# Optimization experiments

Measured on AMD Instinct MI355X. Metric: run time of the kernel, lower is better.

Reference implementation:

```python
import jax, jax.numpy as jnp
import numpy as np

EMBED_DIM = 512
N_QUERY = 4096
N_PROTO = 1024


def setup_inputs() -> dict:
    key = jax.random.key(0)
    k_q, k_p, k_wmu = jax.random.split(key, 3)
    d = EMBED_DIM
    bound = (6.0 / (d + d)) ** 0.5
    return {
        "query_features": jax.random.normal(k_q, (N_QUERY, d), dtype=jnp.float32),
        "prototypes": jax.random.normal(k_p, (N_PROTO, d), dtype=jnp.float32),
        "weight_mu": jax.random.uniform(k_wmu, (d, d), dtype=jnp.float32, minval=-bound, maxval=bound),
        "weight_rho": jnp.full((d, d), -3.0, dtype=jnp.float32),
        "bias_mu": jnp.zeros((d,), dtype=jnp.float32),
        "bias_rho": jnp.full((d,), 0.01, dtype=jnp.float32),
        "n_samples": 10,
    }


def reference(query_features, prototypes, weight_mu, weight_rho, bias_mu, bias_rho, n_samples):
    d = weight_mu.shape[0]
    # softplus reparameterization (same each iteration in the original loop)
    weight_sigma = jnp.log1p(jnp.exp(weight_rho))  # [d, d]
    bias_sigma = jnp.log1p(jnp.exp(bias_rho))      # [d]
    # batched MC weight/bias samples: [S, d, d] and [S, d]
    key = jax.random.key(42)
    kw, kb = jax.random.split(key)
    eps_w = jax.random.normal(kw, (n_samples, d, d), dtype=weight_mu.dtype)
    eps_b = jax.random.normal(kb, (n_samples, d), dtype=bias_mu.dtype)
    w = weight_mu[None] + weight_sigma[None] * eps_w   # [S, d, d]
    b = bias_mu[None] + bias_sigma[None] * eps_b       # [S, d]
    # F.linear(x, W_sample.T, b) == x @ W_sample + b
    tq = jnp.einsum('qd,sde->sqe', query_features, w) + b[:, None, :]  # [S, Q, d]
    # cdist via ||a||^2 + ||b||^2 - 2 a.b
    sq_q = jnp.sum(tq * tq, axis=-1)                    # [S, Q]
    sq_p = jnp.sum(prototypes * prototypes, axis=-1)    # [P]
    cross = jnp.einsum('sqe,pe->sqp', tq, prototypes)   # [S, Q, P]
    sqd = sq_q[:, :, None] + sq_p[None, None, :] - 2.0 * cross
    dists = jnp.sqrt(jnp.maximum(sqd, 1e-12))           # [S, Q, P]
    mean_distance = jnp.mean(dists, axis=0)
    uncertainty = jnp.std(dists, axis=0, ddof=1)        # torch.std is unbiased
    return mean_distance, uncertainty
```

## Files before the change

kernel.cpp:

```cpp
#include <hip/hip_runtime.h>
#include <stdint.h>

#define NS 10
#define DIM 512
#define NQ 4096
#define NP 1024

typedef unsigned short ushort_t;
typedef __bf16 bf16el_t;
typedef bf16el_t bf16x8 __attribute__((ext_vector_type(8)));
typedef float floatx4 __attribute__((ext_vector_type(4)));

__host__ __device__ __forceinline__ uint32_t rotl32(uint32_t x, int r) {
  return (x << r) | (x >> (32 - r));
}

__host__ __device__ __forceinline__ void threefry2x32(uint32_t k0, uint32_t k1,
                                                      uint32_t x0, uint32_t x1,
                                                      uint32_t* o0, uint32_t* o1) {
  uint32_t ks2 = k0 ^ k1 ^ 0x1BD11BDAu;
  x0 += k0; x1 += k1;
#define TF_R(r) { x0 += x1; x1 = rotl32(x1, r); x1 ^= x0; }
  TF_R(13) TF_R(15) TF_R(26) TF_R(6)   x0 += k1;  x1 += ks2 + 1u;
  TF_R(17) TF_R(29) TF_R(16) TF_R(24)  x0 += ks2; x1 += k0 + 2u;
  TF_R(13) TF_R(15) TF_R(26) TF_R(6)   x0 += k0;  x1 += k1 + 3u;
  TF_R(17) TF_R(29) TF_R(16) TF_R(24)  x0 += k1;  x1 += ks2 + 4u;
  TF_R(13) TF_R(15) TF_R(26) TF_R(6)   x0 += ks2; x1 += k0 + 5u;
#undef TF_R
  *o0 = x0; *o1 = x1;
}

__device__ __forceinline__ uint32_t jax_random_bits(uint32_t k0, uint32_t k1, uint32_t idx) {
  uint32_t o0, o1;
  threefry2x32(k0, k1, 0u, idx, &o0, &o1);
  return o0 ^ o1;
}

__device__ __forceinline__ float erfinvf_xla(float x) {
  float w = -log1pf(-x * x);
  float p;
  if (w < 5.0f) {
    w -= 2.5f;
    p = 2.81022636e-08f;
    p = fmaf(p, w, 3.43273939e-07f);
    p = fmaf(p, w, -3.5233877e-06f);
    p = fmaf(p, w, -4.39150654e-06f);
    p = fmaf(p, w, 0.00021858087f);
    p = fmaf(p, w, -0.00125372503f);
    p = fmaf(p, w, -0.00417768164f);
    p = fmaf(p, w, 0.246640727f);
    p = fmaf(p, w, 1.50140941f);
  } else {
    w = sqrtf(w) - 3.0f;
    p = -0.000200214257f;
    p = fmaf(p, w, 0.000100950558f);
    p = fmaf(p, w, 0.00134934322f);
    p = fmaf(p, w, -0.00367342844f);
    p = fmaf(p, w, 0.00573950773f);
    p = fmaf(p, w, -0.0076224613f);
    p = fmaf(p, w, 0.00943887047f);
    p = fmaf(p, w, 1.00167406f);
    p = fmaf(p, w, 2.83297682f);
  }
  return p * x;
}

__device__ __forceinline__ float jax_bits_to_normal(uint32_t bits) {
  float f = __uint_as_float((bits >> 9) | 0x3F800000u) - 1.0f;
  float u = f * 2.0f - 0.99999994f;
  u = fmaxf(u, -0.99999994f);
  return 1.41421356f * erfinvf_xla(u);
}

__device__ __forceinline__ float softplusf(float x) { return log1pf(expf(x)); }

__device__ __forceinline__ float bf2f(ushort_t u) {
  return __uint_as_float(((uint32_t)u) << 16);
}
__device__ __forceinline__ ushort_t f2bf(float f) {
  uint32_t u = __float_as_uint(f);
  u += 0x7FFFu + ((u >> 16) & 1u);
  return (ushort_t)(u >> 16);
}

__device__ __forceinline__ void gll16(const void* g, void* l) {
  __builtin_amdgcn_global_load_lds(
      (const __attribute__((address_space(1))) uint32_t*)g,
      (__attribute__((address_space(3))) uint32_t*)l, 16, 0, 0);
}


__global__ __launch_bounds__(256) void gen_w_kernel(const float* __restrict__ wmu,
                                                    const float* __restrict__ wrho,
                                                    ushort_t* __restrict__ wt,
                                                    uint32_t kw0, uint32_t kw1) {
  uint32_t tid = blockIdx.x * 256u + threadIdx.x;
  uint32_t s = tid >> 18;
  uint32_t r = tid & 0x3FFFFu;
  uint32_t e = r >> 9;
  uint32_t k = r & 511u;
  uint32_t eps_idx = (s << 18) | (k << 9) | e;
  uint32_t bits = jax_random_bits(kw0, kw1, eps_idx);
  float n = jax_bits_to_normal(bits);
  uint32_t mi = (k << 9) | e;
  float w = wmu[mi] + softplusf(wrho[mi]) * n;
  wt[tid] = f2bf(w);
}

__global__ __launch_bounds__(256) void gen_b_kernel(const float* __restrict__ bmu,
                                                    const float* __restrict__ brho,
                                                    float* __restrict__ bvec,
                                                    uint32_t kb0, uint32_t kb1) {
  uint32_t tid = blockIdx.x * 256u + threadIdx.x;
  uint32_t e = tid & 511u;
  uint32_t bits = jax_random_bits(kb0, kb1, tid);
  float n = jax_bits_to_normal(bits);
  bvec[tid] = bmu[e] + softplusf(brho[e]) * n;
}

__global__ __launch_bounds__(256) void cvt_q_kernel(const float* __restrict__ qf,
                                                    ushort_t* __restrict__ qb) {
  int i = (blockIdx.x * 256 + threadIdx.x) * 4;
  float4 v = *(const float4*)&qf[i];
  uint2 r;
  r.x = (uint32_t)f2bf(v.x) | ((uint32_t)f2bf(v.y) << 16);
  r.y = (uint32_t)f2bf(v.z) | ((uint32_t)f2bf(v.w) << 16);
  *(uint2*)&qb[i] = r;
}

__global__ __launch_bounds__(64) void cvt_p_sqp_kernel(const float* __restrict__ pf,
                                                       ushort_t* __restrict__ pb,
                                                       float* __restrict__ sqp) {
  int p = blockIdx.x;
  int lane = threadIdx.x;
  const float* src = pf + p * DIM + lane * 8;
  float4 a = *(const float4*)src;
  float4 b = *(const float4*)(src + 4);
  float vals[8] = {a.x, a.y, a.z, a.w, b.x, b.y, b.z, b.w};
  ushort_t o[8];
  float ss = 0.f;
#pragma unroll
  for (int i = 0; i < 8; ++i) {
    o[i] = f2bf(vals[i]);
    float f = bf2f(o[i]);
    ss += f * f;
  }
  *(uint4*)&pb[p * DIM + lane * 8] = *(const uint4*)o;
#pragma unroll
  for (int off = 32; off; off >>= 1) ss += __shfl_xor(ss, off, 64);
  if (lane == 0) sqp[p] = ss;
}


__global__ __launch_bounds__(256) void gemm_tq_kernel(const ushort_t* __restrict__ qb,
                                                      const ushort_t* __restrict__ wt,
                                                      const float* __restrict__ bvec,
                                                      ushort_t* __restrict__ tq) {
  __shared__ __align__(16) ushort_t lsA[128 * 64];
  __shared__ __align__(16) ushort_t lsB[128 * 64];
  const int lane = threadIdx.x & 63;
  const int wave = threadIdx.x >> 6;
  const int wm = wave >> 1, wn = wave & 1;
  const int qBase = blockIdx.x * 128;
  const int eBase = blockIdx.y * 128;
  const int s = blockIdx.z;
  const ushort_t* wbase = wt + (size_t)s * (DIM * DIM);
  const int srow = lane >> 3;
  const int scol = ((lane & 7) ^ srow) * 16;
  const char* gA = (const char*)qb + (size_t)(qBase + wave * 32 + srow) * (DIM * 2) + scol;
  const char* gB = (const char*)wbase + (size_t)(eBase + wave * 32 + srow) * (DIM * 2) + scol;
  char* lA = (char*)&lsA[wave * 32 * 64];
  char* lB = (char*)&lsB[wave * 32 * 64];
  const int cn = lane & 15;
  const int cn7 = cn & 7;
  const int jc = lane >> 4;
  const floatx4 fzero = {0.f, 0.f, 0.f, 0.f};
  floatx4 acc[4][4];
#pragma unroll
  for (int mi = 0; mi < 4; ++mi)
#pragma unroll
    for (int ni = 0; ni < 4; ++ni) acc[mi][ni] = fzero;

  for (int kt = 0; kt < 8; ++kt) {
    __syncthreads();
#pragma unroll
    for (int j = 0; j < 4; ++j) {
      gll16(gA + (size_t)j * 8 * (DIM * 2), lA + j * 1024);
      gll16(gB + (size_t)j * 8 * (DIM * 2), lB + j * 1024);
    }
    gA += 128; gB += 128;
    __syncthreads();
#pragma unroll
    for (int c = 0; c < 8; c += 4) {
      const int po = ((c + jc) ^ cn7) << 3;
      bf16x8 aF[4], bF[4];
#pragma unroll
      for (int mi = 0; mi < 4; ++mi)
        aF[mi] = *(const bf16x8*)&lsA[(wm * 64 + mi * 16 + cn) * 64 + po];
#pragma unroll
      for (int ni = 0; ni < 4; ++ni)
        bF[ni] = *(const bf16x8*)&lsB[(wn * 64 + ni * 16 + cn) * 64 + po];
#pragma unroll
      for (int mi = 0; mi < 4; ++mi)
#pragma unroll
        for (int ni = 0; ni < 4; ++ni)
          acc[mi][ni] = __builtin_amdgcn_mfma_f32_16x16x32_bf16(aF[mi], bF[ni], acc[mi][ni], 0, 0, 0);
    }
  }
  const int rq = (lane >> 4) * 4;
#pragma unroll
  for (int ni = 0; ni < 4; ++ni) {
    const int e = eBase + wn * 64 + ni * 16 + cn;
    const float bv = bvec[s * DIM + e];
#pragma unroll
    for (int mi = 0; mi < 4; ++mi)
#pragma unroll
      for (int r = 0; r < 4; ++r) {
        const int q = qBase + wm * 64 + mi * 16 + rq + r;
        tq[(size_t)s * (NQ * DIM) + (size_t)q * DIM + e] = f2bf(acc[mi][ni][r] + bv);
      }
  }
}

__global__ __launch_bounds__(256) void sqq_kernel(const ushort_t* __restrict__ tq,
                                                  float* __restrict__ sqq) {
  int tid = blockIdx.x * 256 + threadIdx.x;
  int row = tid >> 4;
  int sub = tid & 15;
  const uint4* rp = (const uint4*)(tq + (size_t)row * DIM);
  float ss = 0.f;
#pragma unroll
  for (int i = 0; i < 4; ++i) {
    uint4 v = rp[sub + i * 16];
    uint32_t wsv[4] = {v.x, v.y, v.z, v.w};
#pragma unroll
    for (int j = 0; j < 4; ++j) {
      float lo = bf2f((ushort_t)(wsv[j] & 0xFFFFu));
      float hi = bf2f((ushort_t)(wsv[j] >> 16));
      ss += lo * lo + hi * hi;
    }
  }
#pragma unroll
  for (int off = 8; off; off >>= 1) ss += __shfl_xor(ss, off, 64);
  if (sub == 0) sqq[row] = ss;
}

__global__ __launch_bounds__(256) void gemm_dist_kernel(const ushort_t* __restrict__ tq,
                                                        const ushort_t* __restrict__ pb,
                                                        const float* __restrict__ sqq,
                                                        const float* __restrict__ sqp,
                                                        float* __restrict__ out) {
  __shared__ __align__(16) ushort_t lsA[64 * 64];
  __shared__ __align__(16) ushort_t lsB[128 * 64];
  const int lane = threadIdx.x & 63;
  const int wave = threadIdx.x >> 6;
  const int wm = wave >> 1;
  const int wn = wave & 1;
  const int qBase = blockIdx.x * 64;
  const int pBase = blockIdx.y * 128;
  const int srow = lane >> 3;
  const int scol = ((lane & 7) ^ srow) * 16;
  const char* gA = (const char*)tq + (size_t)(qBase + wave * 16 + srow) * (DIM * 2) + scol;
  const char* gB = (const char*)pb + (size_t)(pBase + wave * 32 + srow) * (DIM * 2) + scol;
  char* lA = (char*)&lsA[wave * 16 * 64];
  char* lB = (char*)&lsB[wave * 32 * 64];
  const int cn = lane & 15;
  const int cn7 = cn & 7;
  const int jc = lane >> 4;
  const int rq = (lane >> 4) * 4;
  const floatx4 fzero = {0.f, 0.f, 0.f, 0.f};

  float sum[2][4][4] = {};
  float ssq[2][4][4] = {};
  float sqp_v[4];
#pragma unroll
  for (int ni = 0; ni < 4; ++ni) sqp_v[ni] = sqp[pBase + wn * 64 + ni * 16 + cn];

  for (int s = 0; s < NS; ++s) {
    floatx4 acc[2][4];
#pragma unroll
    for (int mi = 0; mi < 2; ++mi)
#pragma unroll
      for (int ni = 0; ni < 4; ++ni) acc[mi][ni] = fzero;

    for (int kt = 0; kt < 8; ++kt) {
      __syncthreads();
      gll16(gA, lA);
      gll16(gA + (size_t)8 * (DIM * 2), lA + 1024);
#pragma unroll
      for (int j = 0; j < 4; ++j)
        gll16(gB + (size_t)j * 8 * (DIM * 2), lB + j * 1024);
      gA += 128; gB += 128;
      __syncthreads();
#pragma unroll
      for (int c = 0; c < 8; c += 4) {
        const int po = ((c + jc) ^ cn7) << 3;
        bf16x8 aF[2], bF[4];
#pragma unroll
        for (int mi = 0; mi < 2; ++mi)
          aF[mi] = *(const bf16x8*)&lsA[(wm * 32 + mi * 16 + cn) * 64 + po];
#pragma unroll
        for (int ni = 0; ni < 4; ++ni)
          bF[ni] = *(const bf16x8*)&lsB[(wn * 64 + ni * 16 + cn) * 64 + po];
#pragma unroll
        for (int mi = 0; mi < 2; ++mi)
#pragma unroll
          for (int ni = 0; ni < 4; ++ni)
            acc[mi][ni] = __builtin_amdgcn_mfma_f32_16x16x32_bf16(aF[mi], bF[ni], acc[mi][ni], 0, 0, 0);
      }
    }
    gA += (size_t)NQ * DIM * 2 - 1024;
    gB -= 1024;
#pragma unroll
    for (int mi = 0; mi < 2; ++mi) {
      float4 aqv = *(const float4*)&sqq[s * NQ + qBase + wm * 32 + mi * 16 + rq];
      float aqa[4] = {aqv.x, aqv.y, aqv.z, aqv.w};
#pragma unroll
      for (int r = 0; r < 4; ++r) {
        float aq = aqa[r];
#pragma unroll
        for (int ni = 0; ni < 4; ++ni) {
          float c = acc[mi][ni][r];
          float dd = sqrtf(fmaxf(aq + sqp_v[ni] - 2.0f * c, 1e-12f));
          sum[mi][ni][r] += dd;
          ssq[mi][ni][r] += dd * dd;
        }
      }
    }
  }
#pragma unroll
  for (int mi = 0; mi < 2; ++mi)
#pragma unroll
    for (int ni = 0; ni < 4; ++ni)
#pragma unroll
      for (int r = 0; r < 4; ++r) {
        int q = qBase + wm * 32 + mi * 16 + rq + r;
        int p = pBase + wn * 64 + ni * 16 + cn;
        float sm = sum[mi][ni][r];
        float mean = sm * 0.1f;
        float var = (ssq[mi][ni][r] - sm * sm * 0.1f) * (1.0f / 9.0f);
        out[(size_t)q * NP + p] = mean;
        out[(size_t)NQ * NP + (size_t)q * NP + p] = sqrtf(fmaxf(var, 0.0f));
      }
}

extern "C" void kernel_launch(void* const* d_in, const int* in_sizes, int n_in,
                              void* d_out, int out_size, void* d_ws, size_t ws_size,
                              hipStream_t stream) {
  const float* qf   = (const float*)d_in[0];
  const float* pf   = (const float*)d_in[1];
  const float* wmu  = (const float*)d_in[2];
  const float* wrho = (const float*)d_in[3];
  const float* bmu  = (const float*)d_in[4];
  const float* brho = (const float*)d_in[5];
  float* out = (float*)d_out;
  char* ws = (char*)d_ws;
  ushort_t* wt   = (ushort_t*)(ws);
  ushort_t* qb   = (ushort_t*)(ws + 5242880);
  ushort_t* pb   = (ushort_t*)(ws + 9437184);
  float*    bvec = (float*)   (ws + 10485760);
  float*    sqp  = (float*)   (ws + 10506240);
  ushort_t* tq   = (ushort_t*)(ws + 10510336);
  float*    sqq  = (float*)   (ws + 52453376);

  uint32_t kw0, kw1, kb0, kb1;
  threefry2x32(0u, 42u, 0u, 0u, &kw0, &kw1);
  threefry2x32(0u, 42u, 0u, 1u, &kb0, &kb1);

  hipLaunchKernelGGL(gen_w_kernel, dim3(10240), dim3(256), 0, stream, wmu, wrho, wt, kw0, kw1);
  hipLaunchKernelGGL(gen_b_kernel, dim3(20), dim3(256), 0, stream, bmu, brho, bvec, kb0, kb1);
  hipLaunchKernelGGL(cvt_q_kernel, dim3(2048), dim3(256), 0, stream, qf, qb);
  hipLaunchKernelGGL(cvt_p_sqp_kernel, dim3(1024), dim3(64), 0, stream, pf, pb, sqp);
  hipLaunchKernelGGL(gemm_tq_kernel, dim3(32, 4, 10), dim3(256), 0, stream, qb, wt, bvec, tq);
  hipLaunchKernelGGL(sqq_kernel, dim3(2560), dim3(256), 0, stream, tq, sqq);
  hipLaunchKernelGGL(gemm_dist_kernel, dim3(64, 8), dim3(256), 0, stream, tq, pb, sqq, sqp, out);
}
```

Baseline: 226.2 us.

## Fuse prep kernels, fold row norms into GEMM epilogue, widen dist K-tile

Merges the bias generation, query/prototype conversion and sqq zeroing into a single prep kernel, which cuts launch count. The tq GEMM epilogue now stages its output tile through swizzled LDS, writes tq with coalesced 16-byte stores, and accumulates the squared row norms with atomics, so the separate sqq pass over tq is gone. The distance GEMM doubles its K tile to 128 with a 16-chunk swizzle, halving the number of barrier iterations at the cost of more LDS. It also accumulates sqd directly instead of squaring the sqrt. The risks are atomic contention across the four e-blocks and lower occupancy from the larger LDS footprint.

```diff
diff --git a/kernel.cpp b/kernel.cpp
--- a/kernel.cpp
+++ b/kernel.cpp
@@ -89,7 +89,6 @@
       (__attribute__((address_space(3))) uint32_t*)l, 16, 0, 0);
 }
 
-
 __global__ __launch_bounds__(256) void gen_w_kernel(const float* __restrict__ wmu,
                                                     const float* __restrict__ wrho,
                                                     ushort_t* __restrict__ wt,
@@ -107,57 +106,64 @@
   wt[tid] = f2bf(w);
 }
 
-__global__ __launch_bounds__(256) void gen_b_kernel(const float* __restrict__ bmu,
-                                                    const float* __restrict__ brho,
-                                                    float* __restrict__ bvec,
-                                                    uint32_t kb0, uint32_t kb1) {
-  uint32_t tid = blockIdx.x * 256u + threadIdx.x;
-  uint32_t e = tid & 511u;
-  uint32_t bits = jax_random_bits(kb0, kb1, tid);
-  float n = jax_bits_to_normal(bits);
-  bvec[tid] = bmu[e] + softplusf(brho[e]) * n;
-}
-
-__global__ __launch_bounds__(256) void cvt_q_kernel(const float* __restrict__ qf,
-                                                    ushort_t* __restrict__ qb) {
-  int i = (blockIdx.x * 256 + threadIdx.x) * 4;
-  float4 v = *(const float4*)&qf[i];
-  uint2 r;
-  r.x = (uint32_t)f2bf(v.x) | ((uint32_t)f2bf(v.y) << 16);
-  r.y = (uint32_t)f2bf(v.z) | ((uint32_t)f2bf(v.w) << 16);
-  *(uint2*)&qb[i] = r;
-}
-
-__global__ __launch_bounds__(64) void cvt_p_sqp_kernel(const float* __restrict__ pf,
-                                                       ushort_t* __restrict__ pb,
-                                                       float* __restrict__ sqp) {
-  int p = blockIdx.x;
-  int lane = threadIdx.x;
-  const float* src = pf + p * DIM + lane * 8;
-  float4 a = *(const float4*)src;
-  float4 b = *(const float4*)(src + 4);
-  float vals[8] = {a.x, a.y, a.z, a.w, b.x, b.y, b.z, b.w};
-  ushort_t o[8];
-  float ss = 0.f;
-#pragma unroll
-  for (int i = 0; i < 8; ++i) {
-    o[i] = f2bf(vals[i]);
-    float f = bf2f(o[i]);
-    ss += f * f;
-  }
-  *(uint4*)&pb[p * DIM + lane * 8] = *(const uint4*)o;
-#pragma unroll
-  for (int off = 32; off; off >>= 1) ss += __shfl_xor(ss, off, 64);
-  if (lane == 0) sqp[p] = ss;
-}
-
+__global__ __launch_bounds__(256) void prep_kernel(const float* __restrict__ qf,
+                                                   const float* __restrict__ pf,
+                                                   const float* __restrict__ bmu,
+                                                   const float* __restrict__ brho,
+                                                   ushort_t* __restrict__ qb,
+                                                   ushort_t* __restrict__ pb,
+                                                   float* __restrict__ sqp,
+                                                   float* __restrict__ bvec,
+                                                   float* __restrict__ sqq,
+                                                   uint32_t kb0, uint32_t kb1) {
+  const int blk = blockIdx.x;
+  const int tid = threadIdx.x;
+  if (blk < 2048) {
+    int i = (blk * 256 + tid) * 4;
+    float4 v = *(const float4*)&qf[i];
+    uint2 r;
+    r.x = (uint32_t)f2bf(v.x) | ((uint32_t)f2bf(v.y) << 16);
+    r.y = (uint32_t)f2bf(v.z) | ((uint32_t)f2bf(v.w) << 16);
+    *(uint2*)&qb[i] = r;
+  } else if (blk < 2304) {
+    int p = (blk - 2048) * 4 + (tid >> 6);
+    int lane = tid & 63;
+    const float* src = pf + p * DIM + lane * 8;
+    float4 a = *(const float4*)src;
+    float4 b = *(const float4*)(src + 4);
+    float vals[8] = {a.x, a.y, a.z, a.w, b.x, b.y, b.z, b.w};
+    ushort_t o[8];
+    float ss = 0.f;
+#pragma unroll
+    for (int i = 0; i < 8; ++i) {
+      o[i] = f2bf(vals[i]);
+      float f = bf2f(o[i]);
+      ss += f * f;
+    }
+    *(uint4*)&pb[p * DIM + lane * 8] = *(const uint4*)o;
+#pragma unroll
+    for (int off = 32; off; off >>= 1) ss += __shfl_xor(ss, off, 64);
+    if (lane == 0) sqp[p] = ss;
+  } else if (blk < 2324) {
+    uint32_t t2 = (blk - 2304) * 256u + tid;
+    uint32_t e = t2 & 511u;
+    uint32_t bits = jax_random_bits(kb0, kb1, t2);
+    float n = jax_bits_to_normal(bits);
+    bvec[t2] = bmu[e] + softplusf(brho[e]) * n;
+  } else {
+    int i = (blk - 2324) * 256 + tid;
+    sqq[i] = 0.f;
+  }
+}
 
 __global__ __launch_bounds__(256) void gemm_tq_kernel(const ushort_t* __restrict__ qb,
                                                       const ushort_t* __restrict__ wt,
                                                       const float* __restrict__ bvec,
-                                                      ushort_t* __restrict__ tq) {
-  __shared__ __align__(16) ushort_t lsA[128 * 64];
-  __shared__ __align__(16) ushort_t lsB[128 * 64];
+                                                      ushort_t* __restrict__ tq,
+                                                      float* __restrict__ sqq) {
+  __shared__ __align__(16) ushort_t ls[2 * 128 * 64];
+  ushort_t* lsA = ls;
+  ushort_t* lsB = ls + 128 * 64;
   const int lane = threadIdx.x & 63;
   const int wave = threadIdx.x >> 6;
   const int wm = wave >> 1, wn = wave & 1;
@@ -207,42 +213,48 @@
           acc[mi][ni] = __builtin_amdgcn_mfma_f32_16x16x32_bf16(aF[mi], bF[ni], acc[mi][ni], 0, 0, 0);
     }
   }
-  const int rq = (lane >> 4) * 4;
-#pragma unroll
-  for (int ni = 0; ni < 4; ++ni) {
-    const int e = eBase + wn * 64 + ni * 16 + cn;
-    const float bv = bvec[s * DIM + e];
-#pragma unroll
-    for (int mi = 0; mi < 4; ++mi)
+
+  __syncthreads();
+  ushort_t* area = ls + wave * 4096;
+  float bv[4];
+#pragma unroll
+  for (int ni = 0; ni < 4; ++ni) bv[ni] = bvec[s * DIM + eBase + wn * 64 + ni * 16 + cn];
+  const int jc4 = jc * 4;
+#pragma unroll
+  for (int mi = 0; mi < 4; ++mi)
+#pragma unroll
+    for (int ni = 0; ni < 4; ++ni)
 #pragma unroll
       for (int r = 0; r < 4; ++r) {
-        const int q = qBase + wm * 64 + mi * 16 + rq + r;
-        tq[(size_t)s * (NQ * DIM) + (size_t)q * DIM + e] = f2bf(acc[mi][ni][r] + bv);
+        const int lr = mi * 16 + jc4 + r;
+        const int lc = ni * 16 + cn;
+        const int off = lr * 64 + (((lc >> 3) ^ (lr & 7)) << 3) + (lc & 7);
+        area[off] = f2bf(acc[mi][ni][r] + bv[ni]);
       }
-  }
-}
-
-__global__ __launch_bounds__(256) void sqq_kernel(const ushort_t* __restrict__ tq,
-                                                  float* __restrict__ sqq) {
-  int tid = blockIdx.x * 256 + threadIdx.x;
-  int row = tid >> 4;
-  int sub = tid & 15;
-  const uint4* rp = (const uint4*)(tq + (size_t)row * DIM);
-  float ss = 0.f;
-#pragma unroll
-  for (int i = 0; i < 4; ++i) {
-    uint4 v = rp[sub + i * 16];
+  __syncthreads();
+  const int rr = lane >> 3;
+  const int ch = lane & 7;
+  const int physc = ch ^ rr;
+  const size_t tqs = (size_t)s * (NQ * DIM);
+#pragma unroll
+  for (int pass = 0; pass < 8; ++pass) {
+    const int lr = pass * 8 + rr;
+    uint4 v = *(const uint4*)&area[lr * 64 + physc * 8];
     uint32_t wsv[4] = {v.x, v.y, v.z, v.w};
-#pragma unroll
-    for (int j = 0; j < 4; ++j) {
-      float lo = bf2f((ushort_t)(wsv[j] & 0xFFFFu));
-      float hi = bf2f((ushort_t)(wsv[j] >> 16));
+    float ss = 0.f;
+#pragma unroll
+    for (int i = 0; i < 4; ++i) {
+      float lo = bf2f((ushort_t)(wsv[i] & 0xFFFFu));
+      float hi = bf2f((ushort_t)(wsv[i] >> 16));
       ss += lo * lo + hi * hi;
     }
-  }
-#pragma unroll
-  for (int off = 8; off; off >>= 1) ss += __shfl_xor(ss, off, 64);
-  if (sub == 0) sqq[row] = ss;
+    ss += __shfl_xor(ss, 1, 64);
+    ss += __shfl_xor(ss, 2, 64);
+    ss += __shfl_xor(ss, 4, 64);
+    const int q = qBase + wm * 64 + lr;
+    *(uint4*)&tq[tqs + (size_t)q * DIM + eBase + wn * 64 + ch * 8] = v;
+    if (ch == 0) atomicAdd(&sqq[s * NQ + q], ss);
+  }
 }
 
 __global__ __launch_bounds__(256) void gemm_dist_kernel(const ushort_t* __restrict__ tq,
@@ -250,24 +262,24 @@
                                                         const float* __restrict__ sqq,
                                                         const float* __restrict__ sqp,
                                                         float* __restrict__ out) {
-  __shared__ __align__(16) ushort_t lsA[64 * 64];
-  __shared__ __align__(16) ushort_t lsB[128 * 64];
+  __shared__ __align__(16) ushort_t lsA[64 * 128];
+  __shared__ __align__(16) ushort_t lsB[128 * 128];
   const int lane = threadIdx.x & 63;
   const int wave = threadIdx.x >> 6;
   const int wm = wave >> 1;
   const int wn = wave & 1;
   const int qBase = blockIdx.x * 64;
   const int pBase = blockIdx.y * 128;
-  const int srow = lane >> 3;
-  const int scol = ((lane & 7) ^ srow) * 16;
-  const char* gA = (const char*)tq + (size_t)(qBase + wave * 16 + srow) * (DIM * 2) + scol;
-  const char* gB = (const char*)pb + (size_t)(pBase + wave * 32 + srow) * (DIM * 2) + scol;
-  char* lA = (char*)&lsA[wave * 16 * 64];
-  char* lB = (char*)&lsB[wave * 32 * 64];
+  const int srow = lane >> 4;
+  const int scc = lane & 15;
+  const int sccx = scc ^ srow;
+  const char* gA = (const char*)tq + (size_t)(qBase + wave * 16 + srow) * (DIM * 2);
+  const char* gB = (const char*)pb + (size_t)(pBase + wave * 32 + srow) * (DIM * 2);
+  char* lA = (char*)lsA + wave * 4096;
+  char* lB = (char*)lsB + wave * 8192;
   const int cn = lane & 15;
-  const int cn7 = cn & 7;
   const int jc = lane >> 4;
-  const int rq = (lane >> 4) * 4;
+  const int rq = jc * 4;
   const floatx4 fzero = {0.f, 0.f, 0.f, 0.f};
 
   float sum[2][4][4] = {};
@@ -283,25 +295,26 @@
 #pragma unroll
       for (int ni = 0; ni < 4; ++ni) acc[mi][ni] = fzero;
 
-    for (int kt = 0; kt < 8; ++kt) {
+    for (int kt = 0; kt < 4; ++kt) {
       __syncthreads();
-      gll16(gA, lA);
-      gll16(gA + (size_t)8 * (DIM * 2), lA + 1024);
-#pragma unroll
-      for (int j = 0; j < 4; ++j)
-        gll16(gB + (size_t)j * 8 * (DIM * 2), lB + j * 1024);
-      gA += 128; gB += 128;
+#pragma unroll
+      for (int g = 0; g < 4; ++g)
+        gll16(gA + (size_t)g * 4 * (DIM * 2) + ((sccx ^ (g * 4)) << 4), lA + g * 1024);
+#pragma unroll
+      for (int g = 0; g < 8; ++g)
+        gll16(gB + (size_t)g * 4 * (DIM * 2) + ((sccx ^ ((g & 3) * 4)) << 4), lB + g * 1024);
+      gA += 256; gB += 256;
       __syncthreads();
 #pragma unroll
-      for (int c = 0; c < 8; c += 4) {
-        const int po = ((c + jc) ^ cn7) << 3;
+      for (int c4 = 0; c4 < 4; ++c4) {
+        const int po = (((c4 * 4 + jc) ^ cn) & 15) << 3;
         bf16x8 aF[2], bF[4];
 #pragma unroll
         for (int mi = 0; mi < 2; ++mi)
-          aF[mi] = *(const bf16x8*)&lsA[(wm * 32 + mi * 16 + cn) * 64 + po];
+          aF[mi] = *(const bf16x8*)&lsA[(wm * 32 + mi * 16 + cn) * 128 + po];
 #pragma unroll
         for (int ni = 0; ni < 4; ++ni)
-          bF[ni] = *(const bf16x8*)&lsB[(wn * 64 + ni * 16 + cn) * 64 + po];
+          bF[ni] = *(const bf16x8*)&lsB[(wn * 64 + ni * 16 + cn) * 128 + po];
 #pragma unroll
         for (int mi = 0; mi < 2; ++mi)
 #pragma unroll
@@ -320,10 +333,9 @@
         float aq = aqa[r];
 #pragma unroll
         for (int ni = 0; ni < 4; ++ni) {
-          float c = acc[mi][ni][r];
-          float dd = sqrtf(fmaxf(aq + sqp_v[ni] - 2.0f * c, 1e-12f));
-          sum[mi][ni][r] += dd;
-          ssq[mi][ni][r] += dd * dd;
+          float sqd = fmaxf(fmaf(-2.0f, acc[mi][ni][r], aq + sqp_v[ni]), 1e-12f);
+          sum[mi][ni][r] += sqrtf(sqd);
+          ssq[mi][ni][r] += sqd;
         }
       }
     }
@@ -368,10 +380,8 @@
   threefry2x32(0u, 42u, 0u, 1u, &kb0, &kb1);
 
   hipLaunchKernelGGL(gen_w_kernel, dim3(10240), dim3(256), 0, stream, wmu, wrho, wt, kw0, kw1);
-  hipLaunchKernelGGL(gen_b_kernel, dim3(20), dim3(256), 0, stream, bmu, brho, bvec, kb0, kb1);
-  hipLaunchKernelGGL(cvt_q_kernel, dim3(2048), dim3(256), 0, stream, qf, qb);
-  hipLaunchKernelGGL(cvt_p_sqp_kernel, dim3(1024), dim3(64), 0, stream, pf, pb, sqp);
-  hipLaunchKernelGGL(gemm_tq_kernel, dim3(32, 4, 10), dim3(256), 0, stream, qb, wt, bvec, tq);
-  hipLaunchKernelGGL(sqq_kernel, dim3(2560), dim3(256), 0, stream, tq, sqq);
+  hipLaunchKernelGGL(prep_kernel, dim3(2484), dim3(256), 0, stream,
+                     qf, pf, bmu, brho, qb, pb, sqp, bvec, sqq, kb0, kb1);
+  hipLaunchKernelGGL(gemm_tq_kernel, dim3(32, 4, 10), dim3(256), 0, stream, qb, wt, bvec, tq, sqq);
   hipLaunchKernelGGL(gemm_dist_kernel, dim3(64, 8), dim3(256), 0, stream, tq, pb, sqq, sqp, out);
 }
```

Result: faster. 210.3 us (-7.1%).
